# Kernel optimization log

Measured on AMD Instinct MI355X. Metric: run time of the kernel, lower is better.

The kernel has to match this reference:

```python
import jax, jax.numpy as jnp
import numpy as np

DIM = 768
N_HEADS = 12
HEAD_DIM = DIM // N_HEADS  # 64
SEQ = 4096
ROPE_THETA = 10000.0  # local layer (layer_id=1)
WINDOW = 128          # local_attention; mask is distance <= WINDOW // 2


def setup_inputs() -> dict:
    key = jax.random.key(0)
    k1, k2, k3 = jax.random.split(key, 3)
    x = jax.random.normal(k1, (1, SEQ, DIM), dtype=jnp.float32)
    position_ids = jnp.arange(SEQ, dtype=jnp.int64 if jax.config.jax_enable_x64 else jnp.int32).reshape(1, SEQ)
    wqkv = jax.random.normal(k2, (3 * DIM, DIM), dtype=jnp.float32) * 0.02
    wo = jax.random.normal(k3, (DIM, DIM), dtype=jnp.float32) * 0.02
    return {"x": x, "position_ids": position_ids, "wqkv": wqkv, "wo": wo}


def _rope_cos_sin(position_ids):
    # inv_freq over even dims, freqs duplicated to full head_dim
    inv_freq = 1.0 / (ROPE_THETA ** (jnp.arange(0, HEAD_DIM, 2, dtype=jnp.float32) / HEAD_DIM))
    pos = position_ids.reshape(-1).astype(jnp.float32)           # [S]
    freqs = pos[:, None] * inv_freq[None, :]                      # [S, hd/2]
    freqs = jnp.concatenate([freqs, freqs], axis=-1)              # [S, hd]
    return jnp.cos(freqs)[None, None], jnp.sin(freqs)[None, None]  # [1,1,S,hd]


def _rotate_half(t):
    h = t.shape[-1] // 2
    return jnp.concatenate([-t[..., h:], t[..., :h]], axis=-1)


def reference(x, position_ids, wqkv, wo):
    bsz, seq_len, _ = x.shape
    qkv = jnp.einsum("bsd,ed->bse", x, wqkv)                      # [B,S,3*dim]
    qkv = qkv.reshape(bsz, seq_len, 3, N_HEADS, HEAD_DIM)
    qkv = jnp.transpose(qkv, (0, 3, 2, 1, 4))                      # [B,H,3,S,hd]
    q, k, v = qkv[:, :, 0], qkv[:, :, 1], qkv[:, :, 2]             # [B,H,S,hd]

    cos, sin = _rope_cos_sin(position_ids)
    q = q * cos + _rotate_half(q) * sin
    k = k * cos + _rotate_half(k) * sin

    scale = HEAD_DIM ** -0.5
    scores = jnp.einsum("bhqd,bhkd->bhqk", q, k) * scale           # [B,H,S,S]

    # sliding-window mask: |i - j| <= WINDOW // 2
    idx = jnp.arange(seq_len)
    dist = jnp.abs(idx[None, :] - idx[:, None])                    # [S,S]
    window_mask = dist <= (WINDOW // 2)
    scores = jnp.where(window_mask[None, None], scores, -jnp.inf)

    attn = jax.nn.softmax(scores, axis=-1)
    out = jnp.einsum("bhqk,bhkd->bhqd", attn, v)                   # [B,H,S,hd]
    out = jnp.transpose(out, (0, 2, 1, 3)).reshape(bsz, seq_len, DIM)
    out = jnp.einsum("bsd,ed->bse", out, wo)
    return out
```

## Files before the change

### kernel.cpp

```cpp
#include <hip/hip_runtime.h>
#include <math.h>

#define SEQ 4096
#define DIM 768
#define NH 12
#define HD 64
#define QKV_N 2304
#define HALF_WIN 64

typedef __attribute__((ext_vector_type(8))) short bf16x8;
typedef __attribute__((ext_vector_type(4))) float floatx4;

__device__ __forceinline__ unsigned short f2bf(float f) {
    unsigned u = __float_as_uint(f);
    unsigned r = (u + 0x7fffu + ((u >> 16) & 1u)) >> 16;
    return (unsigned short)r;
}

__device__ __forceinline__ void gld16(const void* g, void* l) {
    __builtin_amdgcn_global_load_lds(
        (const __attribute__((address_space(1))) unsigned*)g,
        (__attribute__((address_space(3))) unsigned*)l, 16, 0, 0);
}

__device__ __forceinline__ void fast_sc(float x, float* s, float* c) {
    float r = x * 0.15915494309189535f;
    r = r - floorf(r);
    *s = __builtin_amdgcn_sinf(r);
    *c = __builtin_amdgcn_cosf(r);
}

__global__ __launch_bounds__(256) void cast3_bf16(const float* __restrict__ x,
                                                  const float* __restrict__ wqkv,
                                                  const float* __restrict__ wo,
                                                  unsigned short* __restrict__ dst,
                                                  int nx4, int nw4, int ntot4) {
    int i = blockIdx.x * 256 + threadIdx.x;
    if (i >= ntot4) return;
    const float4* src;
    int off;
    if (i < nx4)            { src = (const float4*)x;    off = i; }
    else if (i < nx4 + nw4) { src = (const float4*)wqkv; off = i - nx4; }
    else                    { src = (const float4*)wo;   off = i - nx4 - nw4; }
    float4 v = src[off];
    ushort4 r;
    r.x = f2bf(v.x); r.y = f2bf(v.y); r.z = f2bf(v.z); r.w = f2bf(v.w);
    *(ushort4*)(dst + (size_t)i * 4) = r;
}

__global__ __launch_bounds__(256) void gemm_qkv_rope(const unsigned short* __restrict__ A,
                                                     const unsigned short* __restrict__ B,
                                                     unsigned short* __restrict__ qr,
                                                     unsigned short* __restrict__ kr,
                                                     unsigned short* __restrict__ vt) {
    __shared__ __align__(16) short smem[12288];
    short* As = smem;
    short* Bs = smem + 4096;
    const int t  = threadIdx.x;
    const int wv = t >> 6, ln = t & 63;
    const int wm = wv >> 1, wn = wv & 1;
    const int bm0 = blockIdx.y * 64;
    const int bn0 = blockIdx.x * 128;
    const int lrow = ln >> 3;
    const int lu   = ln & 7;
    const int frow = ln & 15;
    const int q    = ln >> 4;
    const int K = DIM;

    const unsigned short* gptr[6];
    short* lptr[6];
#pragma unroll
    for (int i = 0; i < 6; i++) {
        int idx = wv * 6 + i;
        if (idx < 8) {
            int row = idx * 8 + lrow;
            gptr[i] = A + (size_t)(bm0 + row) * K + ((lu ^ (row & 7)) << 3);
            lptr[i] = As + idx * 512;
        } else {
            int c = idx - 8;
            int row = c * 8 + lrow;
            gptr[i] = B + (size_t)(bn0 + row) * K + ((lu ^ (row & 7)) << 3);
            lptr[i] = Bs + c * 512;
        }
    }

    floatx4 acc[2][4];
#pragma unroll
    for (int i = 0; i < 2; i++)
#pragma unroll
        for (int j = 0; j < 4; j++) acc[i][j] = (floatx4){0.f, 0.f, 0.f, 0.f};

    for (int k0 = 0; k0 < K; k0 += 64) {
        __syncthreads();
#pragma unroll
        for (int i = 0; i < 6; i++) gld16(gptr[i] + k0, (void*)lptr[i]);
        __syncthreads();

#pragma unroll
        for (int ks = 0; ks < 2; ks++) {
            bf16x8 af[2], bfr[4];
#pragma unroll
            for (int mt = 0; mt < 2; mt++) {
                int ra = wm * 32 + mt * 16 + frow;
                af[mt] = *(const bf16x8*)&As[ra * 64 + (((ks * 4 + q) ^ (ra & 7)) << 3)];
            }
#pragma unroll
            for (int nt = 0; nt < 4; nt++) {
                int rb = wn * 64 + nt * 16 + frow;
                bfr[nt] = *(const bf16x8*)&Bs[rb * 64 + (((ks * 4 + q) ^ (rb & 7)) << 3)];
            }
#pragma unroll
            for (int mt = 0; mt < 2; mt++)
#pragma unroll
                for (int nt = 0; nt < 4; nt++)
                    acc[mt][nt] = __builtin_amdgcn_mfma_f32_16x16x32_bf16(
                        af[mt], bfr[nt], acc[mt][nt], 0, 0, 0);
        }
    }

    const int cn = frow;
    const int part = (bn0 >= 1536) ? 2 : (bn0 >= 768 ? 1 : 0);

    if (part < 2) {
        const int colw = bn0 + wn * 64 - part * 768;
        const int h = colw >> 6;
        unsigned short* dst = (part == 0 ? qr : kr) + (size_t)h * SEQ * HD;
        const float invf0 = exp2f(-(float)cn * 0.4152410118609203f);
        const float invf1 = exp2f(-(float)(cn + 16) * 0.4152410118609203f);
#pragma unroll
        for (int mt = 0; mt < 2; mt++) {
            int sbase = bm0 + wm * 32 + mt * 16 + q * 4;
#pragma unroll
            for (int r = 0; r < 4; r++) {
                float ss = (float)(sbase + r);
                float sn0, cs0, sn1, cs1;
                fast_sc(ss * invf0, &sn0, &cs0);
                fast_sc(ss * invf1, &sn1, &cs1);
                float o0 = acc[mt][0][r] * cs0 - acc[mt][2][r] * sn0;
                float o1 = acc[mt][1][r] * cs1 - acc[mt][3][r] * sn1;
                float o2 = acc[mt][2][r] * cs0 + acc[mt][0][r] * sn0;
                float o3 = acc[mt][3][r] * cs1 + acc[mt][1][r] * sn1;
                unsigned short* p = dst + (size_t)(sbase + r) * HD + cn;
                p[0]  = f2bf(o0);
                p[16] = f2bf(o1);
                p[32] = f2bf(o2);
                p[48] = f2bf(o3);
            }
        }
    } else {
        short* vstage = smem;
        __syncthreads();
#pragma unroll
        for (int mt = 0; mt < 2; mt++) {
#pragma unroll
            for (int nt = 0; nt < 4; nt++) {
                int d    = wn * 64 + nt * 16 + cn;
                int sloc = wm * 32 + mt * 16 + q * 4;
                ushort4 pk;
                pk.x = f2bf(acc[mt][nt][0]);
                pk.y = f2bf(acc[mt][nt][1]);
                pk.z = f2bf(acc[mt][nt][2]);
                pk.w = f2bf(acc[mt][nt][3]);
                *(ushort4*)&vstage[d * 72 + sloc] = pk;
            }
        }
        __syncthreads();
        const int dr = t >> 1, sh = (t & 1) * 32;
        const int vcol = bn0 - 1536 + dr;
        unsigned short* vp = vt + (size_t)vcol * SEQ + bm0 + sh;
#pragma unroll
        for (int i = 0; i < 4; i++)
            *(uint4*)(vp + i * 8) = *(const uint4*)&vstage[dr * 72 + sh + i * 8];
    }
}

__global__ __launch_bounds__(256) void gemm_out(const unsigned short* __restrict__ A,
                                                const unsigned short* __restrict__ B,
                                                float* __restrict__ C,
                                                int M, int N, int K) {
    __shared__ __align__(16) short As[64 * 64];
    __shared__ __align__(16) short Bs[64 * 64];
    const int t  = threadIdx.x;
    const int wv = t >> 6, ln = t & 63;
    const int wm = wv >> 1, wn = wv & 1;
    const int bm0 = blockIdx.y * 64;
    const int bn0 = blockIdx.x * 64;
    const int lrow = ln >> 3;
    const int lu   = ln & 7;
    const int frow = ln & 15;
    const int q    = ln >> 4;

    const unsigned short* gptr[4];
    short* lptr[4];
#pragma unroll
    for (int i = 0; i < 4; i++) {
        int idx = wv * 4 + i;
        int c   = (idx < 8) ? idx : idx - 8;
        int row = c * 8 + lrow;
        int g   = (lu ^ (row & 7)) << 3;
        if (idx < 8) {
            gptr[i] = A + (size_t)(bm0 + row) * K + g;
            lptr[i] = As + c * 512;
        } else {
            gptr[i] = B + (size_t)(bn0 + row) * K + g;
            lptr[i] = Bs + c * 512;
        }
    }

    floatx4 acc[2][2];
#pragma unroll
    for (int i = 0; i < 2; i++)
#pragma unroll
        for (int j = 0; j < 2; j++) acc[i][j] = (floatx4){0.f, 0.f, 0.f, 0.f};

    for (int k0 = 0; k0 < K; k0 += 64) {
        __syncthreads();
#pragma unroll
        for (int i = 0; i < 4; i++) gld16(gptr[i] + k0, (void*)lptr[i]);
        __syncthreads();

#pragma unroll
        for (int ks = 0; ks < 2; ks++) {
            bf16x8 af[2], bfr[2];
#pragma unroll
            for (int mt = 0; mt < 2; mt++) {
                int ra = wm * 32 + mt * 16 + frow;
                af[mt] = *(const bf16x8*)&As[ra * 64 + (((ks * 4 + q) ^ (ra & 7)) << 3)];
            }
#pragma unroll
            for (int nt = 0; nt < 2; nt++) {
                int rb = wn * 32 + nt * 16 + frow;
                bfr[nt] = *(const bf16x8*)&Bs[rb * 64 + (((ks * 4 + q) ^ (rb & 7)) << 3)];
            }
#pragma unroll
            for (int mt = 0; mt < 2; mt++)
#pragma unroll
                for (int nt = 0; nt < 2; nt++)
                    acc[mt][nt] = __builtin_amdgcn_mfma_f32_16x16x32_bf16(
                        af[mt], bfr[nt], acc[mt][nt], 0, 0, 0);
        }
    }

    const int cn = ln & 15;
    const int rb4 = (ln >> 4) * 4;
#pragma unroll
    for (int mt = 0; mt < 2; mt++) {
#pragma unroll
        for (int nt = 0; nt < 2; nt++) {
            floatx4 v = acc[mt][nt];
            float* cp = C + (size_t)(bm0 + wm * 32 + mt * 16 + rb4) * N +
                        bn0 + wn * 32 + nt * 16 + cn;
#pragma unroll
            for (int r = 0; r < 4; r++) cp[(size_t)r * N] = v[r];
        }
    }
}

__global__ __launch_bounds__(256) void attn_mfma(const unsigned short* __restrict__ Q,
                                                 const unsigned short* __restrict__ K,
                                                 const unsigned short* __restrict__ Vt,
                                                 unsigned short* __restrict__ Out) {
    __shared__ __align__(16) short lds[16384];
    short* Qs  = lds;
    short* Ks  = lds + 4096;
    short* Vts = lds + 8192;
    short* Pb  = lds + 12288;
    const int t  = threadIdx.x;
    const int wv = t >> 6, ln = t & 63;
    const int h  = blockIdx.x, qs = blockIdx.y * 64;
    const int frow = ln & 15, qd = ln >> 4;
    const int rl = ln >> 3, uu = ln & 7;
    const unsigned short* Qh = Q + (size_t)h * SEQ * HD;
    const unsigned short* Kh = K + (size_t)h * SEQ * HD;
    const unsigned short* Vh = Vt + (size_t)h * HD * SEQ;

#pragma unroll
    for (int i = 0; i < 2; i++) {
        int p = wv * 2 + i;
        int row = p * 8 + rl;
        int g = uu ^ ((row + (row >> 3)) & 7);
        gld16(Qh + (size_t)(qs + row) * 64 + g * 8, (void*)(Qs + p * 512));
    }
    __syncthreads();
    const int arow = wv * 16 + frow;
    const int az = (arow + (arow >> 3)) & 7;
    bf16x8 af0 = *(const bf16x8*)&Qs[arow * 64 + ((qd ^ az) << 3)];
    bf16x8 af1 = *(const bf16x8*)&Qs[arow * 64 + (((qd + 4) ^ az) << 3)];

    floatx4 accO[4];
#pragma unroll
    for (int i = 0; i < 4; i++) accO[i] = (floatx4){0.f, 0.f, 0.f, 0.f};
    float m_r[4] = {-1e30f, -1e30f, -1e30f, -1e30f};
    float l_r[4] = {0.f, 0.f, 0.f, 0.f};

    for (int c = 0; c < 3; c++) {
        const int kb  = qs - 64 + c * 64;
        const int kbc = kb < 0 ? 0 : (kb > SEQ - 64 ? SEQ - 64 : kb);
        __syncthreads();
#pragma unroll
        for (int i = 0; i < 2; i++) {
            int p = wv * 2 + i;
            int row = p * 8 + rl;
            int g = uu ^ ((row + (row >> 3)) & 7);
            gld16(Kh + (size_t)(kbc + row) * 64 + g * 8, (void*)(Ks + p * 512));
            gld16(Vh + (size_t)row * SEQ + kbc + g * 8, (void*)(Vts + p * 512));
        }
        __syncthreads();

        float sv[4][4];
        float cm[4] = {-1e30f, -1e30f, -1e30f, -1e30f};
#pragma unroll
        for (int kt = 0; kt < 4; kt++) {
            bool dead = (c == 0 && kt < wv) || (c == 2 && kt > wv);
            if (!dead) {
                int brow = kt * 16 + frow;
                int bz = (brow + (brow >> 3)) & 7;
                bf16x8 b0 = *(const bf16x8*)&Ks[brow * 64 + ((qd ^ bz) << 3)];
                bf16x8 b1 = *(const bf16x8*)&Ks[brow * 64 + (((qd + 4) ^ bz) << 3)];
                floatx4 z = (floatx4){0.f, 0.f, 0.f, 0.f};
                z = __builtin_amdgcn_mfma_f32_16x16x32_bf16(af0, b0, z, 0, 0, 0);
                z = __builtin_amdgcn_mfma_f32_16x16x32_bf16(af1, b1, z, 0, 0, 0);
                int gk = kb + kt * 16 + frow;
#pragma unroll
                for (int r = 0; r < 4; r++) {
                    int gq = qs + wv * 16 + qd * 4 + r;
                    int dd = gq - gk;
                    bool valid = (gk >= 0) && (gk < SEQ) &&
                                 (dd <= HALF_WIN) && (dd >= -HALF_WIN);
                    float x = valid ? z[r] * 0.125f : -1e30f;
                    sv[kt][r] = x;
                    cm[r] = fmaxf(cm[r], x);
                }
            } else {
#pragma unroll
                for (int r = 0; r < 4; r++) sv[kt][r] = -1e30f;
            }
        }
#pragma unroll
        for (int off = 1; off < 16; off <<= 1)
#pragma unroll
            for (int r = 0; r < 4; r++)
                cm[r] = fmaxf(cm[r], __shfl_xor(cm[r], off, 64));
        float al[4], ls[4];
#pragma unroll
        for (int r = 0; r < 4; r++) {
            float mn = fmaxf(m_r[r], cm[r]);
            al[r] = __expf(m_r[r] - mn);
            m_r[r] = mn;
            ls[r] = 0.f;
        }
        const int qrb = wv * 16 + qd * 4;
#pragma unroll
        for (int kt = 0; kt < 4; kt++) {
            bool dead = (c == 0 && kt < wv) || (c == 2 && kt > wv);
            int klocal = kt * 16 + frow;
            int ku = klocal >> 3;
            if (!dead) {
#pragma unroll
                for (int r = 0; r < 4; r++) {
                    float p = (sv[kt][r] > -1e29f) ? __expf(sv[kt][r] - m_r[r]) : 0.f;
                    ls[r] += p;
                    int qrow = qrb + r;
                    int pz = (qrow + (qrow >> 3)) & 7;
                    Pb[qrow * 64 + ((ku ^ pz) << 3) + (klocal & 7)] = (short)f2bf(p);
                }
            } else {
#pragma unroll
                for (int r = 0; r < 4; r++) {
                    int qrow = qrb + r;
                    int pz = (qrow + (qrow >> 3)) & 7;
                    Pb[qrow * 64 + ((ku ^ pz) << 3) + (klocal & 7)] = 0;
                }
            }
        }
#pragma unroll
        for (int off = 1; off < 16; off <<= 1)
#pragma unroll
            for (int r = 0; r < 4; r++) ls[r] += __shfl_xor(ls[r], off, 64);
#pragma unroll
        for (int r = 0; r < 4; r++) l_r[r] = l_r[r] * al[r] + ls[r];
#pragma unroll
        for (int dt = 0; dt < 4; dt++)
#pragma unroll
            for (int r = 0; r < 4; r++) accO[dt][r] *= al[r];
        __syncthreads();

        const int prow = wv * 16 + frow;
        const int pz2 = (prow + (prow >> 3)) & 7;
        bf16x8 pa0 = *(const bf16x8*)&Pb[prow * 64 + ((qd ^ pz2) << 3)];
        bf16x8 pa1 = *(const bf16x8*)&Pb[prow * 64 + (((qd + 4) ^ pz2) << 3)];
#pragma unroll
        for (int dt = 0; dt < 4; dt++) {
            int vrow = dt * 16 + frow;
            int vz = (vrow + (vrow >> 3)) & 7;
            bf16x8 v0 = *(const bf16x8*)&Vts[vrow * 64 + ((qd ^ vz) << 3)];
            bf16x8 v1 = *(const bf16x8*)&Vts[vrow * 64 + (((qd + 4) ^ vz) << 3)];
            accO[dt] = __builtin_amdgcn_mfma_f32_16x16x32_bf16(pa0, v0, accO[dt], 0, 0, 0);
            accO[dt] = __builtin_amdgcn_mfma_f32_16x16x32_bf16(pa1, v1, accO[dt], 0, 0, 0);
        }
    }

    __syncthreads();
    short* Ob = lds + 4096;
    float linv[4];
#pragma unroll
    for (int r = 0; r < 4; r++) linv[r] = 1.0f / l_r[r];
#pragma unroll
    for (int dt = 0; dt < 4; dt++)
#pragma unroll
        for (int r = 0; r < 4; r++) {
            int qrow = wv * 16 + qd * 4 + r;
            int dcol = dt * 16 + frow;
            Ob[qrow * 72 + dcol] = (short)f2bf(accO[dt][r] * linv[r]);
        }
    __syncthreads();
    const int orow = t >> 2, og = (t & 3) * 16;
    uint4 a = *(const uint4*)&Ob[orow * 72 + og];
    uint4 b = *(const uint4*)&Ob[orow * 72 + og + 8];
    unsigned short* op = Out + (size_t)(qs + orow) * DIM + h * HD + og;
    *(uint4*)(op)     = a;
    *(uint4*)(op + 8) = b;
}

extern "C" void kernel_launch(void* const* d_in, const int* in_sizes, int n_in,
                              void* d_out, int out_size, void* d_ws, size_t ws_size,
                              hipStream_t stream) {
    const float* x    = (const float*)d_in[0];
    const float* wqkv = (const float*)d_in[2];
    const float* wo   = (const float*)d_in[3];
    float* out = (float*)d_out;

    unsigned short* q_r  = (unsigned short*)d_ws;
    unsigned short* k_r  = q_r + (size_t)NH * SEQ * HD;
    unsigned short* v_t  = k_r + (size_t)NH * SEQ * HD;
    unsigned short* x_bf = v_t + (size_t)NH * SEQ * HD;
    unsigned short* wqkv_bf = x_bf + (size_t)SEQ * DIM;
    unsigned short* wo_bf   = wqkv_bf + (size_t)QKV_N * DIM;
    unsigned short* attn_bf = wo_bf + (size_t)DIM * DIM;

    const int nx4 = SEQ * DIM / 4;
    const int nw4 = QKV_N * DIM / 4;
    const int no4 = DIM * DIM / 4;
    const int ntot4 = nx4 + nw4 + no4;

    cast3_bf16<<<dim3((ntot4 + 255) / 256), 256, 0, stream>>>(
        x, wqkv, wo, x_bf, nx4, nw4, ntot4);
    gemm_qkv_rope<<<dim3(QKV_N / 128, SEQ / 64), 256, 0, stream>>>(
        x_bf, wqkv_bf, q_r, k_r, v_t);
    attn_mfma<<<dim3(NH, SEQ / 64), 256, 0, stream>>>(
        q_r, k_r, v_t, attn_bf);
    gemm_out<<<dim3(DIM / 64, SEQ / 64), 256, 0, stream>>>(
        attn_bf, wo_bf, out, SEQ, DIM, DIM);
}
```

Measured before the change: 130.2 us.

## Enlarge attention query tile to 128 rows with 8 waves sharing K/V chunks

The attention kernel now handles 128 queries per block with 512 threads instead of 64 queries with 256 threads. Each block walks four 64-key chunks instead of three, so each K/V chunk staged in LDS serves twice as many queries and global K/V traffic per query drops. Q fragments are loaded straight from global memory into registers, removing the Q LDS stage and one barrier. Per-wave liveness tests skip the QK MFMAs, softmax and PV work for key tiles outside the window. The cost is half as many blocks, which lowers parallelism and occupancy, and more per-wave branching.

```diff
diff --git a/kernel.cpp b/kernel.cpp
--- a/kernel.cpp
+++ b/kernel.cpp
@@ -256,36 +256,26 @@
     }
 }
 
-__global__ __launch_bounds__(256) void attn_mfma(const unsigned short* __restrict__ Q,
+__global__ __launch_bounds__(512) void attn_mfma(const unsigned short* __restrict__ Q,
                                                  const unsigned short* __restrict__ K,
                                                  const unsigned short* __restrict__ Vt,
                                                  unsigned short* __restrict__ Out) {
     __shared__ __align__(16) short lds[16384];
-    short* Qs  = lds;
-    short* Ks  = lds + 4096;
-    short* Vts = lds + 8192;
-    short* Pb  = lds + 12288;
+    short* Ks  = lds;
+    short* Vts = lds + 4096;
+    short* Pb  = lds + 8192;
     const int t  = threadIdx.x;
     const int wv = t >> 6, ln = t & 63;
-    const int h  = blockIdx.x, qs = blockIdx.y * 64;
+    const int h  = blockIdx.x, qs = blockIdx.y * 128;
     const int frow = ln & 15, qd = ln >> 4;
     const int rl = ln >> 3, uu = ln & 7;
     const unsigned short* Qh = Q + (size_t)h * SEQ * HD;
     const unsigned short* Kh = K + (size_t)h * SEQ * HD;
     const unsigned short* Vh = Vt + (size_t)h * HD * SEQ;
 
-#pragma unroll
-    for (int i = 0; i < 2; i++) {
-        int p = wv * 2 + i;
-        int row = p * 8 + rl;
-        int g = uu ^ ((row + (row >> 3)) & 7);
-        gld16(Qh + (size_t)(qs + row) * 64 + g * 8, (void*)(Qs + p * 512));
-    }
-    __syncthreads();
-    const int arow = wv * 16 + frow;
-    const int az = (arow + (arow >> 3)) & 7;
-    bf16x8 af0 = *(const bf16x8*)&Qs[arow * 64 + ((qd ^ az) << 3)];
-    bf16x8 af1 = *(const bf16x8*)&Qs[arow * 64 + (((qd + 4) ^ az) << 3)];
+    const unsigned short* qp = Qh + (size_t)(qs + wv * 16 + frow) * HD;
+    bf16x8 af0 = *(const bf16x8*)(qp + qd * 8);
+    bf16x8 af1 = *(const bf16x8*)(qp + (qd + 4) * 8);
 
     floatx4 accO[4];
 #pragma unroll
@@ -293,115 +283,127 @@
     float m_r[4] = {-1e30f, -1e30f, -1e30f, -1e30f};
     float l_r[4] = {0.f, 0.f, 0.f, 0.f};
 
-    for (int c = 0; c < 3; c++) {
+    const int qlo = wv * 16;
+
+    for (int c = 0; c < 4; c++) {
         const int kb  = qs - 64 + c * 64;
         const int kbc = kb < 0 ? 0 : (kb > SEQ - 64 ? SEQ - 64 : kb);
         __syncthreads();
-#pragma unroll
-        for (int i = 0; i < 2; i++) {
-            int p = wv * 2 + i;
-            int row = p * 8 + rl;
+        {
+            int row = wv * 8 + rl;
             int g = uu ^ ((row + (row >> 3)) & 7);
-            gld16(Kh + (size_t)(kbc + row) * 64 + g * 8, (void*)(Ks + p * 512));
-            gld16(Vh + (size_t)row * SEQ + kbc + g * 8, (void*)(Vts + p * 512));
-        }
-        __syncthreads();
+            gld16(Kh + (size_t)(kbc + row) * HD + g * 8, (void*)(Ks + wv * 512));
+            gld16(Vh + (size_t)row * SEQ + kbc + g * 8, (void*)(Vts + wv * 512));
+        }
+        __syncthreads();
+
+        const int klo0 = c * 64 - 64;
+        bool live_kt[4];
+        bool any_live = false;
+#pragma unroll
+        for (int kt = 0; kt < 4; kt++) {
+            int d0 = qlo - (klo0 + kt * 16);
+            live_kt[kt] = (d0 <= 64) && (d0 >= -64);
+            any_live = any_live || live_kt[kt];
+        }
 
         float sv[4][4];
         float cm[4] = {-1e30f, -1e30f, -1e30f, -1e30f};
-#pragma unroll
-        for (int kt = 0; kt < 4; kt++) {
-            bool dead = (c == 0 && kt < wv) || (c == 2 && kt > wv);
-            if (!dead) {
-                int brow = kt * 16 + frow;
-                int bz = (brow + (brow >> 3)) & 7;
-                bf16x8 b0 = *(const bf16x8*)&Ks[brow * 64 + ((qd ^ bz) << 3)];
-                bf16x8 b1 = *(const bf16x8*)&Ks[brow * 64 + (((qd + 4) ^ bz) << 3)];
-                floatx4 z = (floatx4){0.f, 0.f, 0.f, 0.f};
-                z = __builtin_amdgcn_mfma_f32_16x16x32_bf16(af0, b0, z, 0, 0, 0);
-                z = __builtin_amdgcn_mfma_f32_16x16x32_bf16(af1, b1, z, 0, 0, 0);
-                int gk = kb + kt * 16 + frow;
-#pragma unroll
-                for (int r = 0; r < 4; r++) {
-                    int gq = qs + wv * 16 + qd * 4 + r;
-                    int dd = gq - gk;
-                    bool valid = (gk >= 0) && (gk < SEQ) &&
-                                 (dd <= HALF_WIN) && (dd >= -HALF_WIN);
-                    float x = valid ? z[r] * 0.125f : -1e30f;
-                    sv[kt][r] = x;
-                    cm[r] = fmaxf(cm[r], x);
+        if (any_live) {
+#pragma unroll
+            for (int kt = 0; kt < 4; kt++) {
+                if (live_kt[kt]) {
+                    int brow = kt * 16 + frow;
+                    int bz = (brow + (brow >> 3)) & 7;
+                    bf16x8 b0 = *(const bf16x8*)&Ks[brow * 64 + ((qd ^ bz) << 3)];
+                    bf16x8 b1 = *(const bf16x8*)&Ks[brow * 64 + (((qd + 4) ^ bz) << 3)];
+                    floatx4 z = (floatx4){0.f, 0.f, 0.f, 0.f};
+                    z = __builtin_amdgcn_mfma_f32_16x16x32_bf16(af0, b0, z, 0, 0, 0);
+                    z = __builtin_amdgcn_mfma_f32_16x16x32_bf16(af1, b1, z, 0, 0, 0);
+                    int gk = kb + kt * 16 + frow;
+#pragma unroll
+                    for (int r = 0; r < 4; r++) {
+                        int gq = qs + wv * 16 + qd * 4 + r;
+                        int dd = gq - gk;
+                        bool valid = (gk >= 0) && (gk < SEQ) &&
+                                     (dd <= HALF_WIN) && (dd >= -HALF_WIN);
+                        float x = valid ? z[r] * 0.125f : -1e30f;
+                        sv[kt][r] = x;
+                        cm[r] = fmaxf(cm[r], x);
+                    }
+                } else {
+#pragma unroll
+                    for (int r = 0; r < 4; r++) sv[kt][r] = -1e30f;
                 }
-            } else {
-#pragma unroll
-                for (int r = 0; r < 4; r++) sv[kt][r] = -1e30f;
-            }
-        }
-#pragma unroll
-        for (int off = 1; off < 16; off <<= 1)
-#pragma unroll
-            for (int r = 0; r < 4; r++)
-                cm[r] = fmaxf(cm[r], __shfl_xor(cm[r], off, 64));
-        float al[4], ls[4];
-#pragma unroll
-        for (int r = 0; r < 4; r++) {
-            float mn = fmaxf(m_r[r], cm[r]);
-            al[r] = __expf(m_r[r] - mn);
-            m_r[r] = mn;
-            ls[r] = 0.f;
-        }
-        const int qrb = wv * 16 + qd * 4;
-#pragma unroll
-        for (int kt = 0; kt < 4; kt++) {
-            bool dead = (c == 0 && kt < wv) || (c == 2 && kt > wv);
-            int klocal = kt * 16 + frow;
-            int ku = klocal >> 3;
-            if (!dead) {
-#pragma unroll
-                for (int r = 0; r < 4; r++) {
-                    float p = (sv[kt][r] > -1e29f) ? __expf(sv[kt][r] - m_r[r]) : 0.f;
-                    ls[r] += p;
-                    int qrow = qrb + r;
-                    int pz = (qrow + (qrow >> 3)) & 7;
-                    Pb[qrow * 64 + ((ku ^ pz) << 3) + (klocal & 7)] = (short)f2bf(p);
+            }
+#pragma unroll
+            for (int off = 1; off < 16; off <<= 1)
+#pragma unroll
+                for (int r = 0; r < 4; r++)
+                    cm[r] = fmaxf(cm[r], __shfl_xor(cm[r], off, 64));
+            float al[4], ls[4];
+#pragma unroll
+            for (int r = 0; r < 4; r++) {
+                float mn = fmaxf(m_r[r], cm[r]);
+                al[r] = __expf(m_r[r] - mn);
+                m_r[r] = mn;
+                ls[r] = 0.f;
+            }
+            const int qrb = wv * 16 + qd * 4;
+#pragma unroll
+            for (int kt = 0; kt < 4; kt++) {
+                int klocal = kt * 16 + frow;
+                int ku = klocal >> 3;
+                if (live_kt[kt]) {
+#pragma unroll
+                    for (int r = 0; r < 4; r++) {
+                        float p = (sv[kt][r] > -1e29f) ? __expf(sv[kt][r] - m_r[r]) : 0.f;
+                        ls[r] += p;
+                        int qrow = qrb + r;
+                        int pz = (qrow + (qrow >> 3)) & 7;
+                        Pb[qrow * 64 + ((ku ^ pz) << 3) + (klocal & 7)] = (short)f2bf(p);
+                    }
+                } else {
+#pragma unroll
+                    for (int r = 0; r < 4; r++) {
+                        int qrow = qrb + r;
+                        int pz = (qrow + (qrow >> 3)) & 7;
+                        Pb[qrow * 64 + ((ku ^ pz) << 3) + (klocal & 7)] = 0;
+                    }
                 }
-            } else {
-#pragma unroll
-                for (int r = 0; r < 4; r++) {
-                    int qrow = qrb + r;
-                    int pz = (qrow + (qrow >> 3)) & 7;
-                    Pb[qrow * 64 + ((ku ^ pz) << 3) + (klocal & 7)] = 0;
-                }
-            }
-        }
-#pragma unroll
-        for (int off = 1; off < 16; off <<= 1)
-#pragma unroll
-            for (int r = 0; r < 4; r++) ls[r] += __shfl_xor(ls[r], off, 64);
-#pragma unroll
-        for (int r = 0; r < 4; r++) l_r[r] = l_r[r] * al[r] + ls[r];
-#pragma unroll
-        for (int dt = 0; dt < 4; dt++)
-#pragma unroll
-            for (int r = 0; r < 4; r++) accO[dt][r] *= al[r];
-        __syncthreads();
-
-        const int prow = wv * 16 + frow;
-        const int pz2 = (prow + (prow >> 3)) & 7;
-        bf16x8 pa0 = *(const bf16x8*)&Pb[prow * 64 + ((qd ^ pz2) << 3)];
-        bf16x8 pa1 = *(const bf16x8*)&Pb[prow * 64 + (((qd + 4) ^ pz2) << 3)];
-#pragma unroll
-        for (int dt = 0; dt < 4; dt++) {
-            int vrow = dt * 16 + frow;
-            int vz = (vrow + (vrow >> 3)) & 7;
-            bf16x8 v0 = *(const bf16x8*)&Vts[vrow * 64 + ((qd ^ vz) << 3)];
-            bf16x8 v1 = *(const bf16x8*)&Vts[vrow * 64 + (((qd + 4) ^ vz) << 3)];
-            accO[dt] = __builtin_amdgcn_mfma_f32_16x16x32_bf16(pa0, v0, accO[dt], 0, 0, 0);
-            accO[dt] = __builtin_amdgcn_mfma_f32_16x16x32_bf16(pa1, v1, accO[dt], 0, 0, 0);
+            }
+#pragma unroll
+            for (int off = 1; off < 16; off <<= 1)
+#pragma unroll
+                for (int r = 0; r < 4; r++) ls[r] += __shfl_xor(ls[r], off, 64);
+#pragma unroll
+            for (int r = 0; r < 4; r++) l_r[r] = l_r[r] * al[r] + ls[r];
+#pragma unroll
+            for (int dt = 0; dt < 4; dt++)
+#pragma unroll
+                for (int r = 0; r < 4; r++) accO[dt][r] *= al[r];
+        }
+        __syncthreads();
+
+        if (any_live) {
+            const int prow = wv * 16 + frow;
+            const int pz2 = (prow + (prow >> 3)) & 7;
+            bf16x8 pa0 = *(const bf16x8*)&Pb[prow * 64 + ((qd ^ pz2) << 3)];
+            bf16x8 pa1 = *(const bf16x8*)&Pb[prow * 64 + (((qd + 4) ^ pz2) << 3)];
+#pragma unroll
+            for (int dt = 0; dt < 4; dt++) {
+                int vrow = dt * 16 + frow;
+                int vz = (vrow + (vrow >> 3)) & 7;
+                bf16x8 v0 = *(const bf16x8*)&Vts[vrow * 64 + ((qd ^ vz) << 3)];
+                bf16x8 v1 = *(const bf16x8*)&Vts[vrow * 64 + (((qd + 4) ^ vz) << 3)];
+                accO[dt] = __builtin_amdgcn_mfma_f32_16x16x32_bf16(pa0, v0, accO[dt], 0, 0, 0);
+                accO[dt] = __builtin_amdgcn_mfma_f32_16x16x32_bf16(pa1, v1, accO[dt], 0, 0, 0);
+            }
         }
     }
 
     __syncthreads();
-    short* Ob = lds + 4096;
+    short* Ob = lds;
     float linv[4];
 #pragma unroll
     for (int r = 0; r < 4; r++) linv[r] = 1.0f / l_r[r];
@@ -447,7 +449,7 @@
         x, wqkv, wo, x_bf, nx4, nw4, ntot4);
     gemm_qkv_rope<<<dim3(QKV_N / 128, SEQ / 64), 256, 0, stream>>>(
         x_bf, wqkv_bf, q_r, k_r, v_t);
-    attn_mfma<<<dim3(NH, SEQ / 64), 256, 0, stream>>>(
+    attn_mfma<<<dim3(NH, SEQ / 128), 512, 0, stream>>>(
         q_r, k_r, v_t, attn_bf);
     gemm_out<<<dim3(DIM / 64, SEQ / 64), 256, 0, stream>>>(
         attn_bf, wo_bf, out, SEQ, DIM, DIM);
```

Result: no change. 130.6 us (+0.3%).
